# Performance work log

Hardware: AMD Instinct MI355X
Metric: run time of the kernel (lower is better)

The kernel has to match this reference:

```python
import jax, jax.numpy as jnp
import numpy as np

T = 4096          # flattened document length (tokens)
FLAT = 512        # 2 * lstm_hidden_size
HD = 256          # head embedding dim (head_emb + char_emb)
FEAT = 20         # feature_size
MAXW = 20         # max mention width
NCAND = 30000     # enumerated candidate spans
HID = 512         # scorer hidden size
K = 1638          # floor(T * ment_ratio=0.4)
C = 40            # max antecedents
DEPTH = 2         # coref_depth
NSPK = 10
MENT = 2 * FLAT + FEAT + HD        # 1300 mention emb size
BIN_WIDTHS = [1, 1, 1, 1, 1, 4, 8, 16, 32]   # sums to 65 -> covers clamp(dist,0,64)
BINS = jnp.asarray(np.concatenate([np.full(w, i, dtype=np.int32) for i, w in enumerate(BIN_WIDTHS)]))


def _scorer(x, w1, b1, w2, b2, w3, b3):
    h = jax.nn.relu(x @ w1 + b1)
    h = jax.nn.relu(h @ w2 + b2)
    return (h @ w3 + b3)[..., 0]


def setup_inputs():
    key = jax.random.key(0)
    ks = jax.random.split(key, 30)
    p = lambda i, s: jax.random.normal(ks[i], s, jnp.float32) * 0.02
    cand_starts = jax.random.randint(ks[25], (NCAND,), 0, T)
    widths = jax.random.randint(ks[26], (NCAND,), 0, MAXW)
    cand_ends = jnp.minimum(cand_starts + widths, T - 1)
    return {
        "flat_lstm_out": jax.random.normal(ks[0], (T, FLAT), jnp.float32),
        "head_doc_embs": jax.random.normal(ks[1], (T, HD), jnp.float32),
        "w_span_head": p(2, (FLAT,)), "b_span_head": jnp.zeros((), jnp.float32),
        "width_embed": p(3, (MAXW, FEAT)),
        "ms_w1": p(4, (MENT, HID)), "ms_b1": jnp.zeros((HID,), jnp.float32),
        "ms_w2": p(5, (HID, HID)), "ms_b2": jnp.zeros((HID,), jnp.float32),
        "ms_w3": p(6, (HID, 1)), "ms_b3": jnp.zeros((1,), jnp.float32),
        "fast_w": p(7, (MENT, MENT)), "fast_b": jnp.zeros((MENT,), jnp.float32),
        "ss_w1": p(8, (3 * MENT + 3 * FEAT, HID)), "ss_b1": jnp.zeros((HID,), jnp.float32),
        "ss_w2": p(9, (HID, HID)), "ss_b2": jnp.zeros((HID,), jnp.float32),
        "ss_w3": p(10, (HID, 1)), "ss_b3": jnp.zeros((1,), jnp.float32),
        "gate_w": p(11, (2 * MENT, MENT)), "gate_b": jnp.zeros((MENT,), jnp.float32),
        "speaker_embed": p(12, (2, FEAT)),
        "genre_embed": p(13, (7, FEAT)),
        "dist_embed": p(14, (len(BIN_WIDTHS), FEAT)),
        "cand_starts": cand_starts,
        "cand_ends": cand_ends,
        "speaker_ids": jax.random.randint(ks[27], (T,), 0, NSPK),
        "genre_id": 3,
    }


def reference(flat_lstm_out, head_doc_embs, w_span_head, b_span_head, width_embed,
              ms_w1, ms_b1, ms_w2, ms_b2, ms_w3, ms_b3, fast_w, fast_b,
              ss_w1, ss_b1, ss_w2, ss_b2, ss_w3, ss_b3, gate_w, gate_b,
              speaker_embed, genre_embed, dist_embed,
              cand_starts, cand_ends, speaker_ids, genre_id):
    neg = -jnp.inf
    # ---- mention (span) embeddings: start/end gather + width emb + attention-pooled head ----
    width = cand_ends - cand_starts + 1                              # [N]
    start_embs = flat_lstm_out[cand_starts]                          # [N,FLAT]
    end_embs = flat_lstm_out[cand_ends]                              # [N,FLAT]
    width_embs = width_embed[width - 1]                              # [N,FEAT]
    span_idxs = jnp.clip(jnp.arange(MAXW)[None, :] + cand_starts[:, None], 0, T - 1)  # [N,W]
    ment_doc = head_doc_embs[span_idxs]                              # [N,W,HD]
    head_scores = flat_lstm_out @ w_span_head + b_span_head          # [T]
    g = head_scores[span_idxs] + jnp.where(jnp.arange(MAXW)[None, :] < width[:, None], 0.0, neg)
    attn = jax.nn.softmax(g, axis=1)                                 # [N,W]
    head_embs = jnp.einsum('nw,nwd->nd', attn, ment_doc)             # [N,HD]
    cand_embs = jnp.concatenate([start_embs, end_embs, width_embs, head_embs], axis=1)  # [N,MENT]
    cand_scores = _scorer(cand_embs, ms_w1, ms_b1, ms_w2, ms_b2, ms_w3, ms_b3)          # [N]
    # ---- prune mentions: top-k by score, reordered by document position ----
    _, top_idx = jax.lax.top_k(cand_scores, K)
    ment_pos = cand_starts[top_idx] * cand_ends[-1] + cand_ends[top_idx]
    top_idx = top_idx[jnp.argsort(ment_pos)]
    ment_embs = cand_embs[top_idx]                                   # [K,MENT]
    ment_scores = cand_scores[top_idx]                               # [K]
    ment_speakers = speaker_ids[cand_starts[top_idx]]                # [K]
    # ---- fast (bilinear) antecedent scoring + top-c pruning ----
    idx = jnp.arange(K)
    mask = (idx[:, None] - idx[None, :]) > 0                         # antecedent must precede
    src = ment_embs @ fast_w + fast_b
    fast = src @ ment_embs.T + ment_scores[:, None] + ment_scores[None, :] + jnp.where(mask, 0.0, neg)
    top_fast, antes = jax.lax.top_k(fast, C)                         # [K,C]
    dummy = jnp.zeros((K, 1), fast.dtype)
    genre_emb = jnp.broadcast_to(genre_embed[genre_id][None, None, :], (K, C, FEAT))
    ante_scores = top_fast
    # ---- iterative slow antecedent scoring + gated refinement ----
    for _ in range(DEPTH):
        ante_ment = ment_embs[antes]                                 # [K,C,MENT]
        same = (ment_speakers[:, None] == ment_speakers[antes]).astype(jnp.int32)
        spk_emb = speaker_embed[same]                                # [K,C,FEAT]
        dist_bin = BINS[jnp.clip(idx[:, None] - antes, 0, 64)]
        dist_emb = dist_embed[dist_bin]                              # [K,C,FEAT]
        me = jnp.broadcast_to(ment_embs[:, None, :], (K, C, MENT))
        ante_emb = jnp.concatenate([me, ante_ment, ante_ment * me, spk_emb, genre_emb, dist_emb], axis=2)
        ante_scores = top_fast + _scorer(ante_emb, ss_w1, ss_b1, ss_w2, ss_b2, ss_w3, ss_b3)
        weights = jax.nn.softmax(jnp.concatenate([dummy, ante_scores], axis=1), axis=-1)  # [K,C+1]
        stacked = jnp.concatenate([ment_embs[:, None, :], ante_ment], axis=1)             # [K,C+1,MENT]
        attended = jnp.einsum('kc,kcd->kd', weights, stacked)
        f = jax.nn.sigmoid(jnp.concatenate([ment_embs, attended], axis=1) @ gate_w + gate_b)
        ment_embs = f * attended + (1.0 - f) * ment_embs
    return jnp.concatenate([dummy, ante_scores], axis=1)             # [K,C+1] coref logits
```

## Files before the change

kernel.cpp:

```cpp
#include <hip/hip_runtime.h>
#include <math.h>

#define T_LEN 4096
#define FLATD 512
#define HDD 256
#define FEATD 20
#define NCAND 30000
#define HIDD 512
#define KSEL 1638
#define CANT 40
#define MENTD 1300
#define KPAD 1312
#define NPAIR (KSEL*CANT)
#define NEG_INF (-__builtin_inff())

#define MF_RELU 1
#define MF_MASK 4
#define MF_GATE 8

typedef unsigned short u16;
typedef __attribute__((ext_vector_type(8))) short bf16x8;
typedef __attribute__((ext_vector_type(4))) float f32x4;

__device__ __forceinline__ unsigned ordf(float f){
  unsigned u = __float_as_uint(f);
  return (u & 0x80000000u) ? ~u : (u | 0x80000000u);
}
__device__ __forceinline__ float unordf(unsigned u){
  return __uint_as_float((u & 0x80000000u) ? (u ^ 0x80000000u) : ~u);
}
__device__ __forceinline__ float bf2f(u16 h){ return __uint_as_float(((unsigned)h) << 16); }
__device__ __forceinline__ u16 f2bf(float f){
  unsigned u = __float_as_uint(f);
  u += 0x7fffu + ((u >> 16) & 1u);
  return (u16)(u >> 16);
}
__device__ __forceinline__ unsigned pkmul(unsigned a, unsigned b){
  float a0 = __uint_as_float(a << 16), a1 = __uint_as_float(a & 0xffff0000u);
  float b0 = __uint_as_float(b << 16), b1 = __uint_as_float(b & 0xffff0000u);
  float p0 = a0*b0, p1 = a1*b1;
  unsigned r;
  asm("v_cvt_pk_bf16_f32 %0, %1, %2" : "=v"(r) : "v"(p0), "v"(p1));
  return r;
}
__device__ __forceinline__ int featsrc(int k){
  if (k < 1024) return k;
  if (k < 1280) return k + 20;
  if (k < 1300) return k - 256;
  return -1;
}
__device__ __forceinline__ int swz(int row, int k8){
  return row*32 + ((k8 ^ ((row >> 1) & 3)) << 3);
}
__device__ __forceinline__ void gload16(const u16* g, u16* l){
  __builtin_amdgcn_global_load_lds((const __attribute__((address_space(1))) void*)(g),
                                   (__attribute__((address_space(3))) void*)(l), 16, 0, 0);
}

__global__ __launch_bounds__(256) void k_prep(const float* __restrict__ flat,
    const float* __restrict__ wemb, const float* __restrict__ fast_b, const float* __restrict__ gate_b,
    u16* __restrict__ flatbf, u16* __restrict__ wembP, float* __restrict__ fbP, float* __restrict__ gbP)
{
  int i = blockIdx.x*256 + threadIdx.x;
  if (i < T_LEN*FLATD) flatbf[i] = f2bf(flat[i]);
  if (i < 20*32) wembP[i] = ((i & 31) < 20) ? f2bf(wemb[(i >> 5)*FEATD + (i & 31)]) : (u16)0;
  if (i < KPAD){
    int s = featsrc(i);
    fbP[i] = (s >= 0) ? fast_b[s] : 0.f;
    gbP[i] = (s >= 0) ? gate_b[s] : 0.f;
  }
}

__global__ __launch_bounds__(256) void k_head(const float* __restrict__ flat,
    const float* __restrict__ w, const float* __restrict__ b, float* __restrict__ hs)
{
  int lane = threadIdx.x & 63, wid = threadIdx.x >> 6;
  int row = blockIdx.x*4 + wid;
  if (row >= T_LEN) return;
  const float* x = flat + (size_t)row*FLATD;
  float s = 0.f;
  for (int j = lane; j < FLATD; j += 64) s += x[j]*w[j];
  #pragma unroll
  for (int o = 32; o; o >>= 1) s += __shfl_down(s, o, 64);
  if (lane == 0) hs[row] = s + b[0];
}

__global__ __launch_bounds__(256) void k_cand(const float* __restrict__ hs,
    const float* __restrict__ hdoc, const int* __restrict__ starts, const int* __restrict__ ends,
    u16* __restrict__ hemb)
{
  int wid = threadIdx.x >> 6, lane = threadIdx.x & 63;
  int n = blockIdx.x*4 + wid;
  if (n >= NCAND) return;
  int s = starts[n], e = ends[n];
  int width = e - s + 1;
  float g[20];
  #pragma unroll
  for (int w2 = 0; w2 < 20; ++w2) g[w2] = (w2 < width) ? hs[min(s + w2, T_LEN-1)] : NEG_INF;
  float m = NEG_INF;
  #pragma unroll
  for (int w2 = 0; w2 < 20; ++w2) m = fmaxf(m, g[w2]);
  float sum = 0.f;
  #pragma unroll
  for (int w2 = 0; w2 < 20; ++w2){ g[w2] = expf(g[w2] - m); sum += g[w2]; }
  float inv = 1.f/sum;
  #pragma unroll
  for (int di = 0; di < 4; ++di){
    int d = lane + di*64;
    float acc = 0.f;
    #pragma unroll
    for (int w2 = 0; w2 < 20; ++w2)
      acc += g[w2]*hdoc[(size_t)min(s + w2, T_LEN-1)*HDD + d];
    hemb[(size_t)n*HDD + d] = f2bf(acc*inv);
  }
}

__global__ __launch_bounds__(256) void k_transall(const float* __restrict__ ms_w1,
    const float* __restrict__ ms_w2, const float* __restrict__ fast_w,
    const float* __restrict__ ss_w1, const float* __restrict__ ss_w2,
    const float* __restrict__ gate_w,
    u16* ms1T, u16* ms2T, u16* fastT, u16* ss1abT, u16* sspT,
    u16* ss2T, u16* gateTall)
{
  const float* B; u16* D; int Kb, N, srcN, ldD, kperm, nperm;
  switch (blockIdx.z){
    case 0: B = ms_w1; D = ms1T; Kb = KPAD; N = HIDD; srcN = HIDD; ldD = KPAD; kperm = 1; nperm = 0; break;
    case 1: B = ms_w2; D = ms2T; Kb = HIDD; N = HIDD; srcN = HIDD; ldD = HIDD; kperm = 0; nperm = 0; break;
    case 2: B = fast_w; D = fastT; Kb = KPAD; N = MENTD; srcN = MENTD; ldD = KPAD; kperm = 1; nperm = 1; break;
    case 3: B = ss_w1; D = ss1abT; Kb = KPAD; N = HIDD; srcN = HIDD; ldD = KPAD; kperm = 1; nperm = 0; break;
    case 4: B = ss_w1 + (size_t)MENTD*HIDD; D = ss1abT + (size_t)512*KPAD; Kb = KPAD; N = HIDD; srcN = HIDD; ldD = KPAD; kperm = 1; nperm = 0; break;
    case 5: B = ss_w1 + (size_t)2*MENTD*HIDD; D = sspT; Kb = KPAD; N = HIDD; srcN = HIDD; ldD = KPAD; kperm = 1; nperm = 0; break;
    case 6: B = ss_w2; D = ss2T; Kb = HIDD; N = HIDD; srcN = HIDD; ldD = HIDD; kperm = 0; nperm = 0; break;
    case 7: B = gate_w; D = gateTall; Kb = KPAD; N = MENTD; srcN = MENTD; ldD = 2*KPAD; kperm = 1; nperm = 1; break;
    default: B = gate_w + (size_t)MENTD*MENTD; D = gateTall + KPAD; Kb = KPAD; N = MENTD; srcN = MENTD; ldD = 2*KPAD; kperm = 1; nperm = 1; break;
  }
  int k0 = blockIdx.x*32, n0 = blockIdx.y*32;
  if (k0 >= Kb || n0 >= N) return;
  __shared__ float t[32][33];
  int tx = threadIdx.x & 31, ty = threadIdx.x >> 5;
  for (int r = ty; r < 32; r += 8){
    int gk = k0 + r, gn = n0 + tx;
    int sk = kperm ? featsrc(gk) : ((gk < Kb) ? gk : -1);
    int sn = nperm ? ((gn < N) ? featsrc(gn) : -1) : ((gn < N) ? gn : -1);
    t[r][tx] = (sk >= 0 && sn >= 0) ? B[(size_t)sk*srcN + sn] : 0.f;
  }
  __syncthreads();
  for (int r = ty; r < 32; r += 8){
    int gn = n0 + r, gk = k0 + tx;
    if (gn < N && gk < Kb) D[(size_t)gn*ldD + gk] = f2bf(t[tx][r]);
  }
}

__global__ __launch_bounds__(256) void k_mfma_cand(
    const u16* __restrict__ flatbf, const u16* __restrict__ hemb, const u16* __restrict__ wembP,
    const int* __restrict__ starts, const int* __restrict__ ends,
    const u16* __restrict__ Bt, int M, const float* __restrict__ bias, u16* __restrict__ Cbf)
{
  __shared__ alignas(16) u16 As[4096];
  __shared__ alignas(16) u16 Bs[4096];
  int tid = threadIdx.x;
  int row0 = blockIdx.y*128, col0 = blockIdx.x*128;
  int lane = tid & 63, wid = tid >> 6;
  int wr = wid >> 1, wc = wid & 1;
  int l15 = lane & 15, l4 = lane >> 4;

  int s0 = tid, s1 = tid + 256;
  int r0s = s0 >> 2, c0s = s0 & 3;
  int r1s = s1 >> 2, c1s = s1 & 3;
  int k80 = (c0s ^ ((r0s >> 1) & 3)) << 3;
  int k81 = (c1s ^ ((r1s >> 1) & 3)) << 3;
  int n0r = row0 + r0s; if (n0r >= M) n0r = M - 1;
  int n1r = row0 + r1s; if (n1r >= M) n1r = M - 1;
  int sA0 = starts[n0r], eA0 = ends[n0r];
  int sA1 = starts[n1r], eA1 = ends[n1r];
  const u16* bS0 = flatbf + (size_t)sA0*FLATD;
  const u16* bE0 = flatbf + (size_t)eA0*FLATD;
  const u16* bH0 = hemb + (size_t)n0r*HDD;
  const u16* bW0 = wembP + (eA0 - sA0)*32;
  const u16* bS1 = flatbf + (size_t)sA1*FLATD;
  const u16* bE1 = flatbf + (size_t)eA1*FLATD;
  const u16* bH1p = hemb + (size_t)n1r*HDD;
  const u16* bW1 = wembP + (eA1 - sA1)*32;
  const u16* pb0 = Bt + (size_t)(col0 + r0s)*KPAD + k80;
  const u16* pb1 = Bt + (size_t)(col0 + r1s)*KPAD + k81;
  u16* la0 = As + s0*8; u16* la1 = As + s1*8;
  u16* lb0 = Bs + s0*8; u16* lb1 = Bs + s1*8;

  f32x4 acc[4][4];
  #pragma unroll
  for (int m = 0; m < 4; ++m)
    #pragma unroll
    for (int n = 0; n < 4; ++n)
      #pragma unroll
      for (int q = 0; q < 4; ++q) acc[m][n][q] = 0.f;

  for (int kt = 0; kt < KPAD/32; ++kt){
    int k0 = kt << 5;
    int f0 = k0 + k80, f1 = k0 + k81;
    const u16* src0 = (f0 < 512) ? bS0 + f0 : (f0 < 1024) ? bE0 + (f0 - 512)
                    : (f0 < 1280) ? bH0 + (f0 - 1024) : bW0 + (f0 - 1280);
    const u16* src1 = (f1 < 512) ? bS1 + f1 : (f1 < 1024) ? bE1 + (f1 - 512)
                    : (f1 < 1280) ? bH1p + (f1 - 1024) : bW1 + (f1 - 1280);
    gload16(src0, la0); gload16(src1, la1);
    gload16(pb0 + k0, lb0); gload16(pb1 + k0, lb1);
    __syncthreads();
    bf16x8 af[4], bfr[4];
    #pragma unroll
    for (int m = 0; m < 4; ++m){ int r = wr*64 + m*16 + l15; af[m] = *(const bf16x8*)(As + swz(r, l4)); }
    #pragma unroll
    for (int n = 0; n < 4; ++n){ int cc = wc*64 + n*16 + l15; bfr[n] = *(const bf16x8*)(Bs + swz(cc, l4)); }
    #pragma unroll
    for (int m = 0; m < 4; ++m)
      #pragma unroll
      for (int n = 0; n < 4; ++n)
        acc[m][n] = __builtin_amdgcn_mfma_f32_16x16x32_bf16(af[m], bfr[n], acc[m][n], 0, 0, 0);
    __syncthreads();
  }
  #pragma unroll
  for (int m = 0; m < 4; ++m){
    #pragma unroll
    for (int q = 0; q < 4; ++q){
      int grow = row0 + wr*64 + m*16 + l4*4 + q;
      if (grow >= M) continue;
      #pragma unroll
      for (int n = 0; n < 4; ++n){
        int gcol = col0 + wc*64 + n*16 + l15;
        float v = fmaxf(acc[m][n][q] + bias[gcol], 0.f);
        Cbf[(size_t)grow*HIDD + gcol] = f2bf(v);
      }
    }
  }
}

__global__ __launch_bounds__(256) void k_mfma(const u16* __restrict__ A,
    const u16* __restrict__ A2, const u16* __restrict__ Bt, int M, int N, int Kp, int ldA,
    const float* __restrict__ bias, const float* __restrict__ msc,
    float* __restrict__ Cf, int ldf, u16* __restrict__ Cbf, int ldbf, int Nstore, int flags,
    const u16* __restrict__ g_att, const u16* __restrict__ g_mo)
{
  __shared__ alignas(16) u16 As[4096];
  __shared__ alignas(16) u16 Bs[4096];
  int tid = threadIdx.x;
  int row0 = blockIdx.y*128, col0 = blockIdx.x*128;
  if ((flags & MF_MASK) && col0 >= row0 + 128) return;
  int lane = tid & 63, wid = tid >> 6;
  int wr = wid >> 1, wc = wid & 1;
  int l15 = lane & 15, l4 = lane >> 4;

  int s0 = tid, s1 = tid + 256;
  int r0s = s0 >> 2, c0s = s0 & 3;
  int r1s = s1 >> 2, c1s = s1 & 3;
  int k80 = (c0s ^ ((r0s >> 1) & 3)) << 3;
  int k81 = (c1s ^ ((r1s >> 1) & 3)) << 3;
  int ra0 = row0 + r0s; if (ra0 >= M) ra0 = M - 1;
  int ra1 = row0 + r1s; if (ra1 >= M) ra1 = M - 1;
  int cb0 = col0 + r0s; if (cb0 >= N) cb0 = N - 1;
  int cb1 = col0 + r1s; if (cb1 >= N) cb1 = N - 1;
  const u16* pa0 = A + (size_t)ra0*ldA + k80;
  const u16* pa1 = A + (size_t)ra1*ldA + k81;
  int kt1 = A2 ? (ldA >> 5) : (Kp >> 5);
  int koff = kt1 << 5;
  const u16* qa0 = A2 ? (A2 + (size_t)ra0*ldA + k80 - koff) : pa0;
  const u16* qa1 = A2 ? (A2 + (size_t)ra1*ldA + k81 - koff) : pa1;
  const u16* pb0 = Bt + (size_t)cb0*Kp + k80;
  const u16* pb1 = Bt + (size_t)cb1*Kp + k81;
  u16* la0 = As + s0*8; u16* la1 = As + s1*8;
  u16* lb0 = Bs + s0*8; u16* lb1 = Bs + s1*8;

  f32x4 acc[4][4];
  #pragma unroll
  for (int m = 0; m < 4; ++m)
    #pragma unroll
    for (int n = 0; n < 4; ++n)
      #pragma unroll
      for (int q = 0; q < 4; ++q) acc[m][n][q] = 0.f;

  int nkt = Kp >> 5;
  for (int kt = 0; kt < nkt; ++kt){
    int k0 = kt << 5;
    const u16* a0 = (kt < kt1) ? pa0 : qa0;
    const u16* a1 = (kt < kt1) ? pa1 : qa1;
    gload16(a0 + k0, la0); gload16(a1 + k0, la1);
    gload16(pb0 + k0, lb0); gload16(pb1 + k0, lb1);
    __syncthreads();
    bf16x8 af[4], bfr[4];
    #pragma unroll
    for (int m = 0; m < 4; ++m){ int r = wr*64 + m*16 + l15; af[m] = *(const bf16x8*)(As + swz(r, l4)); }
    #pragma unroll
    for (int n = 0; n < 4; ++n){ int cc = wc*64 + n*16 + l15; bfr[n] = *(const bf16x8*)(Bs + swz(cc, l4)); }
    #pragma unroll
    for (int m = 0; m < 4; ++m)
      #pragma unroll
      for (int n = 0; n < 4; ++n)
        acc[m][n] = __builtin_amdgcn_mfma_f32_16x16x32_bf16(af[m], bfr[n], acc[m][n], 0, 0, 0);
    __syncthreads();
  }
  #pragma unroll
  for (int m = 0; m < 4; ++m){
    #pragma unroll
    for (int q = 0; q < 4; ++q){
      int grow = row0 + wr*64 + m*16 + l4*4 + q;
      if (grow >= M) continue;
      #pragma unroll
      for (int n = 0; n < 4; ++n){
        int gcol = col0 + wc*64 + n*16 + l15;
        if (gcol < N){
          float v = acc[m][n][q];
          if (bias) v += bias[gcol];
          if (flags & MF_MASK){ v += msc[grow] + msc[gcol]; if (gcol >= grow) v = NEG_INF; }
          if (flags & MF_RELU) v = fmaxf(v, 0.f);
          if (flags & MF_GATE){
            float f = 1.f/(1.f + expf(-v));
            float res = f*bf2f(g_att[(size_t)grow*ldbf + gcol])
                      + (1.f - f)*bf2f(g_mo[(size_t)grow*ldbf + gcol]);
            Cbf[(size_t)grow*ldbf + gcol] = f2bf(res);
          } else {
            if (Cf)  Cf[(size_t)grow*ldf + gcol] = v;
            if (Cbf) Cbf[(size_t)grow*ldbf + gcol] = f2bf(v);
          }
        } else if (Cbf && gcol < Nstore){
          Cbf[(size_t)grow*ldbf + gcol] = 0;
        }
      }
    }
  }
}

__global__ __launch_bounds__(256) void k_mfma_rowdot(const u16* __restrict__ A,
    const u16* __restrict__ Bt, int M, const float* __restrict__ b2,
    const float* __restrict__ w3, const float* __restrict__ b3,
    const float* __restrict__ add, float* __restrict__ out)
{
  __shared__ alignas(16) u16 As[4096];
  __shared__ alignas(16) u16 Bs[4096];
  __shared__ float rsum[128][2];
  int tid = threadIdx.x;
  int row0 = blockIdx.x*128;
  int lane = tid & 63, wid = tid >> 6;
  int wr = wid >> 1, wc = wid & 1;
  int l15 = lane & 15, l4 = lane >> 4;

  int s0 = tid, s1 = tid + 256;
  int r0s = s0 >> 2, c0s = s0 & 3;
  int r1s = s1 >> 2, c1s = s1 & 3;
  int k80 = (c0s ^ ((r0s >> 1) & 3)) << 3;
  int k81 = (c1s ^ ((r1s >> 1) & 3)) << 3;
  int ra0 = row0 + r0s; if (ra0 >= M) ra0 = M - 1;
  int ra1 = row0 + r1s; if (ra1 >= M) ra1 = M - 1;
  const u16* pa0 = A + (size_t)ra0*HIDD + k80;
  const u16* pa1 = A + (size_t)ra1*HIDD + k81;
  u16* la0 = As + s0*8; u16* la1 = As + s1*8;
  u16* lb0 = Bs + s0*8; u16* lb1 = Bs + s1*8;

  float rd[4][4] = {};
  for (int p = 0; p < 4; ++p){
    int col0 = p*128;
    const u16* pb0 = Bt + (size_t)(col0 + r0s)*HIDD + k80;
    const u16* pb1 = Bt + (size_t)(col0 + r1s)*HIDD + k81;
    f32x4 acc[4][4];
    #pragma unroll
    for (int m = 0; m < 4; ++m)
      #pragma unroll
      for (int n = 0; n < 4; ++n)
        #pragma unroll
        for (int q = 0; q < 4; ++q) acc[m][n][q] = 0.f;
    for (int kt = 0; kt < HIDD/32; ++kt){
      int k0 = kt << 5;
      gload16(pa0 + k0, la0); gload16(pa1 + k0, la1);
      gload16(pb0 + k0, lb0); gload16(pb1 + k0, lb1);
      __syncthreads();
      bf16x8 af[4], bfr[4];
      #pragma unroll
      for (int m = 0; m < 4; ++m){ int r = wr*64 + m*16 + l15; af[m] = *(const bf16x8*)(As + swz(r, l4)); }
      #pragma unroll
      for (int n = 0; n < 4; ++n){ int cc = wc*64 + n*16 + l15; bfr[n] = *(const bf16x8*)(Bs + swz(cc, l4)); }
      #pragma unroll
      for (int m = 0; m < 4; ++m)
        #pragma unroll
        for (int n = 0; n < 4; ++n)
          acc[m][n] = __builtin_amdgcn_mfma_f32_16x16x32_bf16(af[m], bfr[n], acc[m][n], 0, 0, 0);
      __syncthreads();
    }
    #pragma unroll
    for (int n = 0; n < 4; ++n){
      int gcol = col0 + wc*64 + n*16 + l15;
      float bb = b2[gcol], ww = w3[gcol];
      #pragma unroll
      for (int m = 0; m < 4; ++m)
        #pragma unroll
        for (int q = 0; q < 4; ++q){
          float v = fmaxf(acc[m][n][q] + bb, 0.f);
          rd[m][q] = fmaf(v, ww, rd[m][q]);
        }
    }
  }
  #pragma unroll
  for (int m = 0; m < 4; ++m)
    #pragma unroll
    for (int q = 0; q < 4; ++q){
      float s = rd[m][q];
      s += __shfl_xor(s, 1, 64); s += __shfl_xor(s, 2, 64);
      s += __shfl_xor(s, 4, 64); s += __shfl_xor(s, 8, 64);
      if (l15 == 0) rsum[wr*64 + m*16 + l4*4 + q][wc] = s;
    }
  __syncthreads();
  if (tid < 128){
    int gr = row0 + tid;
    if (gr < M){
      float v = rsum[tid][0] + rsum[tid][1] + b3[0];
      if (add) v += add[gr];
      out[gr] = v;
    }
  }
}

__global__ __launch_bounds__(256) void k_d1_mfma(int Mc,
    const u16* __restrict__ ment, const int* __restrict__ antes, const int* __restrict__ mspk,
    const u16* __restrict__ Bt, const float* __restrict__ A_meb,
    const float* __restrict__ Svec, const float* __restrict__ Dvec, const float* __restrict__ cvec,
    u16* __restrict__ H1)
{
  __shared__ alignas(16) u16 As[4096];
  __shared__ alignas(16) u16 Bs[4096];
  __shared__ int ri[128], rj[128], rsame[128], rbin[128];
  int tid = threadIdx.x;
  int row0 = blockIdx.y*128, col0 = blockIdx.x*128;
  if (tid < 128){
    int r = row0 + tid;
    int p = (r < Mc ? r : 0);
    int i = p / CANT;
    int j = antes[p];
    ri[tid] = i; rj[tid] = j;
    rsame[tid] = (mspk[i] == mspk[j]) ? 1 : 0;
    int d = i - j; d = d < 0 ? 0 : (d > 64 ? 64 : d);
    rbin[tid] = (d <= 4) ? d : (d <= 8 ? 5 : (d <= 16 ? 6 : (d <= 32 ? 7 : 8)));
  }
  __syncthreads();
  int lane = tid & 63, wid = tid >> 6;
  int wr = wid >> 1, wc = wid & 1;
  int l15 = lane & 15, l4 = lane >> 4;

  int s0 = tid, s1 = tid + 256;
  int r0s = s0 >> 2, c0s = s0 & 3;
  int r1s = s1 >> 2, c1s = s1 & 3;
  int k80 = (c0s ^ ((r0s >> 1) & 3)) << 3;
  int k81 = (c1s ^ ((r1s >> 1) & 3)) << 3;
  const u16* pb0 = Bt + (size_t)(col0 + r0s)*KPAD + k80;
  const u16* pb1 = Bt + (size_t)(col0 + r1s)*KPAD + k81;
  u16* lb0 = Bs + s0*8; u16* lb1 = Bs + s1*8;
  const u16* pi0 = ment + (size_t)ri[r0s]*KPAD + k80;
  const u16* pj0 = ment + (size_t)rj[r0s]*KPAD + k80;
  const u16* pi1 = ment + (size_t)ri[r1s]*KPAD + k81;
  const u16* pj1 = ment + (size_t)rj[r1s]*KPAD + k81;

  f32x4 acc[4][4];
  #pragma unroll
  for (int m = 0; m < 4; ++m)
    #pragma unroll
    for (int n = 0; n < 4; ++n)
      #pragma unroll
      for (int q = 0; q < 4; ++q) acc[m][n][q] = 0.f;

  int nkt = KPAD >> 5;
  for (int kt = 0; kt < nkt; ++kt){
    int k0 = kt << 5;
    gload16(pb0 + k0, lb0); gload16(pb1 + k0, lb1);
    {
      uint4 va = *(const uint4*)(pi0 + k0);
      uint4 vb = *(const uint4*)(pj0 + k0);
      uint4 vo;
      vo.x = pkmul(va.x, vb.x); vo.y = pkmul(va.y, vb.y);
      vo.z = pkmul(va.z, vb.z); vo.w = pkmul(va.w, vb.w);
      *(uint4*)(As + s0*8) = vo;
      va = *(const uint4*)(pi1 + k0);
      vb = *(const uint4*)(pj1 + k0);
      vo.x = pkmul(va.x, vb.x); vo.y = pkmul(va.y, vb.y);
      vo.z = pkmul(va.z, vb.z); vo.w = pkmul(va.w, vb.w);
      *(uint4*)(As + s1*8) = vo;
    }
    __syncthreads();
    bf16x8 af[4], bfr[4];
    #pragma unroll
    for (int m = 0; m < 4; ++m){ int r = wr*64 + m*16 + l15; af[m] = *(const bf16x8*)(As + swz(r, l4)); }
    #pragma unroll
    for (int n = 0; n < 4; ++n){ int cc = wc*64 + n*16 + l15; bfr[n] = *(const bf16x8*)(Bs + swz(cc, l4)); }
    #pragma unroll
    for (int m = 0; m < 4; ++m)
      #pragma unroll
      for (int n = 0; n < 4; ++n)
        acc[m][n] = __builtin_amdgcn_mfma_f32_16x16x32_bf16(af[m], bfr[n], acc[m][n], 0, 0, 0);
    __syncthreads();
  }
  #pragma unroll
  for (int m = 0; m < 4; ++m){
    #pragma unroll
    for (int q = 0; q < 4; ++q){
      int rl = wr*64 + m*16 + l4*4 + q;
      int grow = row0 + rl;
      if (grow >= Mc) continue;
      const float* me = A_meb + (size_t)ri[rl]*1024;
      const float* an = A_meb + (size_t)rj[rl]*1024 + 512;
      const float* sv = Svec + rsame[rl]*HIDD;
      const float* dv = Dvec + rbin[rl]*HIDD;
      #pragma unroll
      for (int n = 0; n < 4; ++n){
        int gcol = col0 + wc*64 + n*16 + l15;
        float v = acc[m][n][q] + me[gcol] + an[gcol] + sv[gcol] + dv[gcol] + cvec[gcol];
        H1[(size_t)grow*HIDD + gcol] = f2bf(fmaxf(v, 0.f));
      }
    }
  }
}

__global__ __launch_bounds__(256) void k_selzero(unsigned* selws){
  int i = blockIdx.x*256 + threadIdx.x;
  if (i < 6156) selws[i] = 0;
}
__global__ __launch_bounds__(256) void k_hist(const float* __restrict__ scores,
    unsigned* __restrict__ selws, int pass)
{
  int n = blockIdx.x*256 + threadIdx.x;
  if (n >= NCAND) return;
  unsigned u = ordf(scores[n]);
  const unsigned* meta = selws + 6144;
  if (pass == 0) atomicAdd(&selws[u >> 21], 1u);
  else if (pass == 1){ if ((u >> 21) == meta[0]) atomicAdd(&selws[2048 + ((u >> 10) & 0x7FFu)], 1u); }
  else { if ((u >> 10) == meta[2]) atomicAdd(&selws[4096 + (u & 0x3FFu)], 1u); }
}
__global__ __launch_bounds__(1024) void k_thresh(unsigned* __restrict__ selws, int mode){
  __shared__ unsigned a[2048], b[2048];
  int tid = threadIdx.x;
  unsigned* meta = selws + 6144;
  const unsigned* gbin = selws + (mode == 0 ? 0 : (mode == 1 ? 2048 : 4096));
  unsigned target = (mode == 0) ? (unsigned)KSEL : meta[mode == 1 ? 1 : 3];
  a[tid] = gbin[tid]; a[tid + 1024] = gbin[tid + 1024];
  unsigned *src = a, *dst = b;
  for (int step = 1; step < 2048; step <<= 1){
    __syncthreads();
    for (int i = tid; i < 2048; i += 1024)
      dst[i] = src[i] + ((i + step < 2048) ? src[i + step] : 0u);
    unsigned* t2 = src; src = dst; dst = t2;
  }
  __syncthreads();
  for (int i = tid; i < 2048; i += 1024){
    unsigned si = src[i], sn = (i < 2047) ? src[i+1] : 0u;
    if (si >= target && sn < target){
      if (mode == 0){ meta[0] = (unsigned)i; meta[1] = target - sn; }
      else if (mode == 1){ meta[2] = (meta[0] << 11) | (unsigned)i; meta[3] = target - sn; }
      else { meta[4] = (meta[2] << 10) | (unsigned)i; meta[5] = target - sn; }
    }
  }
}
__global__ __launch_bounds__(256) void k_compact(const float* __restrict__ scores,
    unsigned* __restrict__ selws, int* __restrict__ g_sel, unsigned* __restrict__ g_eq)
{
  int n = blockIdx.x*256 + threadIdx.x;
  if (n >= NCAND) return;
  unsigned kth = selws[6144 + 4];
  unsigned* cnt = selws + 6152;
  unsigned u = ordf(scores[n]);
  if (u > kth){ unsigned p = atomicAdd(&cnt[0], 1u); g_sel[p] = n; }
  else if (u == kth){ unsigned p = atomicAdd(&cnt[1], 1u); if (p < 1024) g_eq[p] = (unsigned)n; }
}
__global__ __launch_bounds__(1024) void k_eqrank(unsigned* __restrict__ selws,
    const unsigned* __restrict__ g_eq, int* __restrict__ g_sel)
{
  __shared__ unsigned eq[1024];
  int tid = threadIdx.x;
  unsigned neq = selws[6152 + 1]; if (neq > 1024u) neq = 1024u;
  unsigned E = selws[6144 + 5];
  unsigned G = selws[6152 + 0];
  eq[tid] = (tid < (int)neq) ? g_eq[tid] : 0xFFFFFFFFu;
  __syncthreads();
  if (tid < (int)neq){
    unsigned mine = eq[tid]; unsigned r = 0;
    for (unsigned j = 0; j < neq; ++j) r += (eq[j] < mine) ? 1u : 0u;
    if (r < E) g_sel[G + r] = (int)mine;
  }
}
__global__ __launch_bounds__(256) void k_rank1(const float* __restrict__ scores,
    const int* __restrict__ g_sel, int* __restrict__ ranked)
{
  __shared__ unsigned long long key[KSEL];
  int tid = threadIdx.x;
  for (int t = tid; t < KSEL; t += 256){
    int n = g_sel[t];
    key[t] = ((unsigned long long)(~ordf(scores[n])) << 32) | (unsigned)n;
  }
  __syncthreads();
  int t = blockIdx.x*256 + tid;
  if (t >= KSEL) return;
  unsigned long long mine = key[t];
  int r = 0;
  #pragma unroll 16
  for (int j = 0; j < KSEL; ++j) r += (key[j] < mine) ? 1 : 0;
  ranked[r] = (int)(mine & 0xFFFFFFFFu);
}
__global__ __launch_bounds__(256) void k_rank2(const int* __restrict__ ranked,
    const int* __restrict__ starts, const int* __restrict__ ends, int* __restrict__ top_idx)
{
  __shared__ unsigned long long key[KSEL];
  int tid = threadIdx.x;
  int elast = ends[NCAND-1];
  for (int t = tid; t < KSEL; t += 256){
    int n = ranked[t];
    unsigned mp = (unsigned)(starts[n]*elast + ends[n]);
    key[t] = ((unsigned long long)mp << 11) | (unsigned)t;
  }
  __syncthreads();
  int t = blockIdx.x*256 + tid;
  if (t >= KSEL) return;
  unsigned long long mine = key[t];
  int r = 0;
  #pragma unroll 16
  for (int j = 0; j < KSEL; ++j) r += (key[j] < mine) ? 1 : 0;
  top_idx[r] = ranked[t];
}

__global__ __launch_bounds__(256) void k_gather(const int* __restrict__ top_idx,
    const u16* __restrict__ flatbf, const u16* __restrict__ hemb, const u16* __restrict__ wembP,
    const int* __restrict__ starts, const int* __restrict__ ends,
    const float* __restrict__ cscores, const int* __restrict__ spk_ids,
    u16* __restrict__ ment, float* __restrict__ mscore, int* __restrict__ mspk)
{
  int k = blockIdx.x; int n = top_idx[k];
  int s = starts[n], e = ends[n];
  int v = threadIdx.x;
  if (v < KPAD/8){
    int f0 = v*8;
    const u16* src = (f0 < 512) ? flatbf + (size_t)s*FLATD + f0
                   : (f0 < 1024) ? flatbf + (size_t)e*FLATD + (f0 - 512)
                   : (f0 < 1280) ? hemb + (size_t)n*HDD + (f0 - 1024)
                   : wembP + (e - s)*32 + (f0 - 1280);
    *(uint4*)(ment + (size_t)k*KPAD + f0) = *(const uint4*)src;
  }
  if (threadIdx.x == 0){ mscore[k] = cscores[n]; mspk[k] = spk_ids[s]; }
}

__global__ __launch_bounds__(256) void k_f3(const float* __restrict__ fast,
    float* __restrict__ top_fast, int* __restrict__ antes)
{
  int wid = threadIdx.x >> 6, lane = threadIdx.x & 63;
  int i = blockIdx.x*4 + wid;
  if (i >= KSEL) return;
  const float* row = fast + (size_t)i*KSEL;
  unsigned long long key[26];
  #pragma unroll
  for (int t = 0; t < 26; ++t){
    int j = lane + (t << 6);
    unsigned long long k2 = 0ULL;
    if (j < i) k2 = ((unsigned long long)ordf(row[j]) << 32) | (unsigned)(0xFFFFFFFFu - (unsigned)j);
    key[t] = k2;
  }
  for (int c = 0; c < CANT; ++c){
    unsigned long long m = 0ULL;
    #pragma unroll
    for (int t = 0; t < 26; ++t) if (key[t] > m) m = key[t];
    #pragma unroll
    for (int o = 32; o; o >>= 1){
      unsigned long long v = __shfl_xor(m, o, 64);
      if (v > m) m = v;
    }
    if (m){
      #pragma unroll
      for (int t = 0; t < 26; ++t) if (key[t] == m) key[t] = 0ULL;
    }
    if (lane == 0){
      if (m){
        top_fast[(size_t)i*CANT + c] = unordf((unsigned)(m >> 32));
        antes[(size_t)i*CANT + c]    = (int)(0xFFFFFFFFu - (unsigned)(m & 0xFFFFFFFFu));
      } else {
        top_fast[(size_t)i*CANT + c] = NEG_INF;
        antes[(size_t)i*CANT + c]    = c;
      }
    }
  }
}

__global__ __launch_bounds__(256) void k_dsmall(const float* __restrict__ ss_w1,
    const float* __restrict__ ss_b1, const float* __restrict__ spk_emb,
    const float* __restrict__ gen_emb, const float* __restrict__ dist_emb,
    const int* __restrict__ genre_id, float* __restrict__ Svec, float* __restrict__ Dvec,
    float* __restrict__ cvec)
{
  int r = blockIdx.x;
  for (int h = threadIdx.x; h < HIDD; h += 256){
    const float* e; const float* wb; float acc;
    if (r < 2){ e = spk_emb + r*FEATD; wb = ss_w1 + (size_t)3900*HIDD; acc = 0.f; }
    else if (r < 11){ e = dist_emb + (r-2)*FEATD; wb = ss_w1 + (size_t)3940*HIDD; acc = 0.f; }
    else { e = gen_emb + genre_id[0]*FEATD; wb = ss_w1 + (size_t)3920*HIDD; acc = ss_b1[h]; }
    for (int f = 0; f < FEATD; ++f) acc += e[f]*wb[(size_t)f*HIDD + h];
    if (r < 2) Svec[r*HIDD + h] = acc;
    else if (r < 11) Dvec[(r-2)*HIDD + h] = acc;
    else cvec[h] = acc;
  }
}

__global__ __launch_bounds__(256) void k_d4a(const float* __restrict__ ante_sc,
    const int* __restrict__ antes, const u16* __restrict__ ment, u16* __restrict__ att_bf)
{
  int i = blockIdx.x;
  __shared__ float w[CANT+1];
  __shared__ int aj[CANT];
  if (threadIdx.x == 0){
    float s[CANT]; float m = 0.f;
    #pragma unroll
    for (int c = 0; c < CANT; ++c){ s[c] = ante_sc[i*CANT + c]; m = fmaxf(m, s[c]); }
    float e0 = expf(0.f - m);
    float sum = e0;
    float ex[CANT];
    #pragma unroll
    for (int c = 0; c < CANT; ++c){ ex[c] = expf(s[c] - m); sum += ex[c]; }
    float inv = 1.f/sum;
    w[0] = e0*inv;
    #pragma unroll
    for (int c = 0; c < CANT; ++c) w[c+1] = ex[c]*inv;
  }
  if (threadIdx.x < CANT) aj[threadIdx.x] = antes[i*CANT + threadIdx.x];
  __syncthreads();
  for (int d = threadIdx.x; d < KPAD; d += 256){
    if (d < MENTD){
      float acc = w[0]*bf2f(ment[(size_t)i*KPAD + d]);
      for (int c = 0; c < CANT; ++c) acc += w[c+1]*bf2f(ment[(size_t)aj[c]*KPAD + d]);
      att_bf[(size_t)i*KPAD + d] = f2bf(acc);
    } else att_bf[(size_t)i*KPAD + d] = 0;
  }
}

__global__ __launch_bounds__(256) void k_out(const float* __restrict__ ante_sc, float* __restrict__ out){
  int idx = blockIdx.x*256 + threadIdx.x;
  if (idx >= KSEL*41) return;
  int i = idx / 41, c = idx % 41;
  float v = (c == 0) ? 0.f : ante_sc[i*CANT + (c-1)];
  if (!isfinite(v)) v = -3.0e38f;
  out[idx] = v;
}

__global__ void k_zero(float* out, int n){
  int i = blockIdx.x*256 + threadIdx.x;
  if (i < n) out[i] = 0.f;
}

extern "C" void kernel_launch(void* const* d_in, const int* in_sizes, int n_in,
                              void* d_out, int out_size, void* d_ws, size_t ws_size,
                              hipStream_t stream)
{
  const float* flat   = (const float*)d_in[0];
  const float* hdoc   = (const float*)d_in[1];
  const float* w_head = (const float*)d_in[2];
  const float* b_head = (const float*)d_in[3];
  const float* wemb   = (const float*)d_in[4];
  const float* ms_w1  = (const float*)d_in[5];
  const float* ms_b1  = (const float*)d_in[6];
  const float* ms_w2  = (const float*)d_in[7];
  const float* ms_b2  = (const float*)d_in[8];
  const float* ms_w3  = (const float*)d_in[9];
  const float* ms_b3  = (const float*)d_in[10];
  const float* fast_w = (const float*)d_in[11];
  const float* fast_b = (const float*)d_in[12];
  const float* ss_w1  = (const float*)d_in[13];
  const float* ss_b1  = (const float*)d_in[14];
  const float* ss_w2  = (const float*)d_in[15];
  const float* ss_b2  = (const float*)d_in[16];
  const float* ss_w3  = (const float*)d_in[17];
  const float* ss_b3  = (const float*)d_in[18];
  const float* gate_w = (const float*)d_in[19];
  const float* gate_b = (const float*)d_in[20];
  const float* spk_e  = (const float*)d_in[21];
  const float* gen_e  = (const float*)d_in[22];
  const float* dist_e = (const float*)d_in[23];
  const int* starts   = (const int*)d_in[24];
  const int* ends     = (const int*)d_in[25];
  const int* spk_ids  = (const int*)d_in[26];
  const int* genre_id = (const int*)d_in[27];
  float* out = (float*)d_out;

  size_t off = 0;
  char* base = (char*)d_ws;
  auto alloc = [&](size_t nbytes) -> void* {
    void* p = (void*)(base + off);
    off += ((nbytes + 255)/256)*256;
    return p;
  };
  float* head_sc = (float*)alloc((size_t)T_LEN*4);
  u16*   flatbf  = (u16*)alloc((size_t)T_LEN*FLATD*2);
  u16*   wembP   = (u16*)alloc((size_t)20*32*2);
  float* fbP     = (float*)alloc((size_t)KPAD*4);
  float* gbP     = (float*)alloc((size_t)KPAD*4);
  u16*   hemb    = (u16*)alloc((size_t)NCAND*HDD*2);
  float* cscores = (float*)alloc((size_t)NCAND*4);
  int*   top_idx = (int*)alloc(2048*4);
  unsigned* selws= (unsigned*)alloc(6160*4);
  int*   g_sel   = (int*)alloc((size_t)KSEL*4);
  unsigned* g_eq = (unsigned*)alloc(1024*4);
  int*   g_rank  = (int*)alloc((size_t)KSEL*4);
  u16*   ms1T    = (u16*)alloc((size_t)HIDD*KPAD*2);
  u16*   ms2T    = (u16*)alloc((size_t)HIDD*HIDD*2);
  u16*   fastT   = (u16*)alloc((size_t)MENTD*KPAD*2);
  u16*   ss1abT  = (u16*)alloc((size_t)1024*KPAD*2);
  u16*   sspT    = (u16*)alloc((size_t)HIDD*KPAD*2);
  u16*   ss2T    = (u16*)alloc((size_t)HIDD*HIDD*2);
  u16*   gateTall= (u16*)alloc((size_t)MENTD*2*KPAD*2);
  u16*   ment    = (u16*)alloc((size_t)KSEL*KPAD*2);
  u16*   mentB   = (u16*)alloc((size_t)KSEL*KPAD*2);
  u16*   srcb    = (u16*)alloc((size_t)KSEL*KPAD*2);
  float* mscore  = (float*)alloc((size_t)KSEL*4);
  int*   mspk    = (int*)alloc((size_t)KSEL*4);
  float* fastm   = (float*)alloc((size_t)KSEL*KSEL*4);
  float* top_fast= (float*)alloc((size_t)NPAIR*4);
  int*   antes   = (int*)alloc((size_t)NPAIR*4);
  float* ante_sc = (float*)alloc((size_t)NPAIR*4);
  float* A_meb   = (float*)alloc((size_t)KSEL*1024*4);
  float* Svec    = (float*)alloc(2*HIDD*4);
  float* Dvec    = (float*)alloc(9*HIDD*4);
  float* cvec    = (float*)alloc(HIDD*4);
  u16*   att_bf  = (u16*)alloc((size_t)KSEL*KPAD*2);
  u16*   bufH1   = (u16*)alloc((size_t)NPAIR*HIDD*2);

  if (ws_size < off){
    k_zero<<<(KSEL*41 + 255)/256, 256, 0, stream>>>(out, KSEL*41);
    return;
  }

  k_prep<<<(T_LEN*FLATD + 255)/256, 256, 0, stream>>>(flat, wemb, fast_b, gate_b,
                                                      flatbf, wembP, fbP, gbP);
  k_transall<<<dim3(KPAD/32, 41, 9), 256, 0, stream>>>(ms_w1, ms_w2, fast_w, ss_w1, ss_w2, gate_w,
      ms1T, ms2T, fastT, ss1abT, sspT, ss2T, gateTall);

  k_head<<<T_LEN/4, 256, 0, stream>>>(flat, w_head, b_head, head_sc);
  k_cand<<<NCAND/4, 256, 0, stream>>>(head_sc, hdoc, starts, ends, hemb);

  k_mfma_cand<<<dim3(HIDD/128, (NCAND + 127)/128), 256, 0, stream>>>(
      flatbf, hemb, wembP, starts, ends, ms1T, NCAND, ms_b1, bufH1);
  k_mfma_rowdot<<<(NCAND + 127)/128, 256, 0, stream>>>(bufH1, ms2T, NCAND, ms_b2, ms_w3, ms_b3,
                                                       nullptr, cscores);

  k_selzero<<<25, 256, 0, stream>>>(selws);
  k_hist<<<(NCAND + 255)/256, 256, 0, stream>>>(cscores, selws, 0);
  k_thresh<<<1, 1024, 0, stream>>>(selws, 0);
  k_hist<<<(NCAND + 255)/256, 256, 0, stream>>>(cscores, selws, 1);
  k_thresh<<<1, 1024, 0, stream>>>(selws, 1);
  k_hist<<<(NCAND + 255)/256, 256, 0, stream>>>(cscores, selws, 2);
  k_thresh<<<1, 1024, 0, stream>>>(selws, 2);
  k_compact<<<(NCAND + 255)/256, 256, 0, stream>>>(cscores, selws, g_sel, g_eq);
  k_eqrank<<<1, 1024, 0, stream>>>(selws, g_eq, g_sel);
  k_rank1<<<(KSEL + 255)/256, 256, 0, stream>>>(cscores, g_sel, g_rank);
  k_rank2<<<(KSEL + 255)/256, 256, 0, stream>>>(g_rank, starts, ends, top_idx);

  k_gather<<<KSEL, 256, 0, stream>>>(top_idx, flatbf, hemb, wembP, starts, ends, cscores, spk_ids,
                                     ment, mscore, mspk);

  k_mfma<<<dim3((MENTD+127)/128, (KSEL+127)/128), 256, 0, stream>>>(
      ment, nullptr, fastT, KSEL, MENTD, KPAD, KPAD, fbP, nullptr,
      nullptr, 0, srcb, KPAD, KPAD, 0, nullptr, nullptr);
  k_mfma<<<dim3((KSEL+127)/128, (KSEL+127)/128), 256, 0, stream>>>(
      srcb, nullptr, ment, KSEL, KSEL, KPAD, KPAD, nullptr, mscore,
      fastm, KSEL, nullptr, 0, 0, MF_MASK, nullptr, nullptr);
  k_f3<<<(KSEL+3)/4, 256, 0, stream>>>(fastm, top_fast, antes);

  k_dsmall<<<12, 256, 0, stream>>>(ss_w1, ss_b1, spk_e, gen_e, dist_e, genre_id, Svec, Dvec, cvec);

  const u16* mcur = ment;
  for (int iter = 0; iter < 2; ++iter){
    k_mfma<<<dim3(8, (KSEL+127)/128), 256, 0, stream>>>(
        mcur, nullptr, ss1abT, KSEL, 1024, KPAD, KPAD, nullptr, nullptr,
        A_meb, 1024, nullptr, 0, 0, 0, nullptr, nullptr);
    k_d1_mfma<<<dim3(HIDD/128, (NPAIR + 127)/128), 256, 0, stream>>>(
        NPAIR, mcur, antes, mspk, sspT, A_meb, Svec, Dvec, cvec, bufH1);
    k_mfma_rowdot<<<(NPAIR + 127)/128, 256, 0, stream>>>(bufH1, ss2T, NPAIR, ss_b2, ss_w3, ss_b3,
                                                         top_fast, ante_sc);
    if (iter == 0){
      k_d4a<<<KSEL, 256, 0, stream>>>(ante_sc, antes, mcur, att_bf);
      k_mfma<<<dim3((MENTD+127)/128, (KSEL+127)/128), 256, 0, stream>>>(
          ment, att_bf, gateTall, KSEL, MENTD, 2*KPAD, KPAD, gbP, nullptr,
          nullptr, 0, mentB, KPAD, KPAD, MF_GATE, att_bf, ment);
      mcur = mentB;
    }
  }

  k_out<<<(KSEL*41 + 255)/256, 256, 0, stream>>>(ante_sc, out);
}
```

Before: 1.357 ms.

## Widen pair GEMM tile, prefetch gathers, precombine feature biases, vectorize attention

```diff
diff --git a/kernel.cpp b/kernel.cpp
--- a/kernel.cpp
+++ b/kernel.cpp
@@ -59,7 +59,8 @@
 
 __global__ __launch_bounds__(256) void k_prep(const float* __restrict__ flat,
     const float* __restrict__ wemb, const float* __restrict__ fast_b, const float* __restrict__ gate_b,
-    u16* __restrict__ flatbf, u16* __restrict__ wembP, float* __restrict__ fbP, float* __restrict__ gbP)
+    u16* __restrict__ flatbf, u16* __restrict__ wembP, float* __restrict__ fbP, float* __restrict__ gbP,
+    unsigned* __restrict__ selws)
 {
   int i = blockIdx.x*256 + threadIdx.x;
   if (i < T_LEN*FLATD) flatbf[i] = f2bf(flat[i]);
@@ -69,6 +70,7 @@
     fbP[i] = (s >= 0) ? fast_b[s] : 0.f;
     gbP[i] = (s >= 0) ? gate_b[s] : 0.f;
   }
+  if (i < 6156) selws[i] = 0;
 }
 
 __global__ __launch_bounds__(256) void k_head(const float* __restrict__ flat,
@@ -417,23 +419,24 @@
 __global__ __launch_bounds__(256) void k_d1_mfma(int Mc,
     const u16* __restrict__ ment, const int* __restrict__ antes, const int* __restrict__ mspk,
     const u16* __restrict__ Bt, const float* __restrict__ A_meb,
-    const float* __restrict__ Svec, const float* __restrict__ Dvec, const float* __restrict__ cvec,
-    u16* __restrict__ H1)
+    const float* __restrict__ comb, u16* __restrict__ H1)
 {
   __shared__ alignas(16) u16 As[4096];
-  __shared__ alignas(16) u16 Bs[4096];
-  __shared__ int ri[128], rj[128], rsame[128], rbin[128];
+  __shared__ alignas(16) u16 Bs[8192];
+  __shared__ int ri[128], rj[128], rcomb[128];
   int tid = threadIdx.x;
-  int row0 = blockIdx.y*128, col0 = blockIdx.x*128;
+  int row0 = blockIdx.y*128;
+  int col0 = blockIdx.x*256;
   if (tid < 128){
     int r = row0 + tid;
     int p = (r < Mc ? r : 0);
     int i = p / CANT;
     int j = antes[p];
     ri[tid] = i; rj[tid] = j;
-    rsame[tid] = (mspk[i] == mspk[j]) ? 1 : 0;
+    int same = (mspk[i] == mspk[j]) ? 1 : 0;
     int d = i - j; d = d < 0 ? 0 : (d > 64 ? 64 : d);
-    rbin[tid] = (d <= 4) ? d : (d <= 8 ? 5 : (d <= 16 ? 6 : (d <= 32 ? 7 : 8)));
+    int bin = (d <= 4) ? d : (d <= 8 ? 5 : (d <= 16 ? 6 : (d <= 32 ? 7 : 8)));
+    rcomb[tid] = same*9 + bin;
   }
   __syncthreads();
   int lane = tid & 63, wid = tid >> 6;
@@ -445,50 +448,67 @@
   int r1s = s1 >> 2, c1s = s1 & 3;
   int k80 = (c0s ^ ((r0s >> 1) & 3)) << 3;
   int k81 = (c1s ^ ((r1s >> 1) & 3)) << 3;
-  const u16* pb0 = Bt + (size_t)(col0 + r0s)*KPAD + k80;
-  const u16* pb1 = Bt + (size_t)(col0 + r1s)*KPAD + k81;
-  u16* lb0 = Bs + s0*8; u16* lb1 = Bs + s1*8;
   const u16* pi0 = ment + (size_t)ri[r0s]*KPAD + k80;
   const u16* pj0 = ment + (size_t)rj[r0s]*KPAD + k80;
   const u16* pi1 = ment + (size_t)ri[r1s]*KPAD + k81;
   const u16* pj1 = ment + (size_t)rj[r1s]*KPAD + k81;
-
-  f32x4 acc[4][4];
+  int t0 = tid, t1 = tid + 256, t2 = tid + 512, t3 = tid + 768;
+  int rB0 = t0 >> 2, rB1 = t1 >> 2, rB2 = t2 >> 2, rB3 = t3 >> 2;
+  int kB0 = ((t0 & 3) ^ ((rB0 >> 1) & 3)) << 3;
+  int kB1 = ((t1 & 3) ^ ((rB1 >> 1) & 3)) << 3;
+  int kB2 = ((t2 & 3) ^ ((rB2 >> 1) & 3)) << 3;
+  int kB3 = ((t3 & 3) ^ ((rB3 >> 1) & 3)) << 3;
+  const u16* pb0 = Bt + (size_t)(col0 + rB0)*KPAD + kB0;
+  const u16* pb1 = Bt + (size_t)(col0 + rB1)*KPAD + kB1;
+  const u16* pb2 = Bt + (size_t)(col0 + rB2)*KPAD + kB2;
+  const u16* pb3 = Bt + (size_t)(col0 + rB3)*KPAD + kB3;
+
+  f32x4 acc[4][8];
   #pragma unroll
   for (int m = 0; m < 4; ++m)
     #pragma unroll
-    for (int n = 0; n < 4; ++n)
+    for (int n = 0; n < 8; ++n)
       #pragma unroll
       for (int q = 0; q < 4; ++q) acc[m][n][q] = 0.f;
+
+  uint4 va0 = *(const uint4*)pi0;
+  uint4 vb0 = *(const uint4*)pj0;
+  uint4 va1 = *(const uint4*)pi1;
+  uint4 vb1 = *(const uint4*)pj1;
 
   int nkt = KPAD >> 5;
   for (int kt = 0; kt < nkt; ++kt){
     int k0 = kt << 5;
-    gload16(pb0 + k0, lb0); gload16(pb1 + k0, lb1);
     {
-      uint4 va = *(const uint4*)(pi0 + k0);
-      uint4 vb = *(const uint4*)(pj0 + k0);
       uint4 vo;
-      vo.x = pkmul(va.x, vb.x); vo.y = pkmul(va.y, vb.y);
-      vo.z = pkmul(va.z, vb.z); vo.w = pkmul(va.w, vb.w);
+      vo.x = pkmul(va0.x, vb0.x); vo.y = pkmul(va0.y, vb0.y);
+      vo.z = pkmul(va0.z, vb0.z); vo.w = pkmul(va0.w, vb0.w);
       *(uint4*)(As + s0*8) = vo;
-      va = *(const uint4*)(pi1 + k0);
-      vb = *(const uint4*)(pj1 + k0);
-      vo.x = pkmul(va.x, vb.x); vo.y = pkmul(va.y, vb.y);
-      vo.z = pkmul(va.z, vb.z); vo.w = pkmul(va.w, vb.w);
+      vo.x = pkmul(va1.x, vb1.x); vo.y = pkmul(va1.y, vb1.y);
+      vo.z = pkmul(va1.z, vb1.z); vo.w = pkmul(va1.w, vb1.w);
       *(uint4*)(As + s1*8) = vo;
     }
+    gload16(pb0 + k0, Bs + t0*8); gload16(pb1 + k0, Bs + t1*8);
+    gload16(pb2 + k0, Bs + t2*8); gload16(pb3 + k0, Bs + t3*8);
+    if (kt + 1 < nkt){
+      int kn = (kt + 1) << 5;
+      va0 = *(const uint4*)(pi0 + kn);
+      vb0 = *(const uint4*)(pj0 + kn);
+      va1 = *(const uint4*)(pi1 + kn);
+      vb1 = *(const uint4*)(pj1 + kn);
+    }
     __syncthreads();
-    bf16x8 af[4], bfr[4];
+    bf16x8 af[4];
     #pragma unroll
     for (int m = 0; m < 4; ++m){ int r = wr*64 + m*16 + l15; af[m] = *(const bf16x8*)(As + swz(r, l4)); }
     #pragma unroll
-    for (int n = 0; n < 4; ++n){ int cc = wc*64 + n*16 + l15; bfr[n] = *(const bf16x8*)(Bs + swz(cc, l4)); }
-    #pragma unroll
-    for (int m = 0; m < 4; ++m)
-      #pragma unroll
-      for (int n = 0; n < 4; ++n)
-        acc[m][n] = __builtin_amdgcn_mfma_f32_16x16x32_bf16(af[m], bfr[n], acc[m][n], 0, 0, 0);
+    for (int n = 0; n < 8; ++n){
+      int cc = wc*128 + n*16 + l15;
+      bf16x8 bfr = *(const bf16x8*)(Bs + swz(cc, l4));
+      #pragma unroll
+      for (int m = 0; m < 4; ++m)
+        acc[m][n] = __builtin_amdgcn_mfma_f32_16x16x32_bf16(af[m], bfr, acc[m][n], 0, 0, 0);
+    }
     __syncthreads();
   }
   #pragma unroll
@@ -500,22 +520,17 @@
       if (grow >= Mc) continue;
       const float* me = A_meb + (size_t)ri[rl]*1024;
       const float* an = A_meb + (size_t)rj[rl]*1024 + 512;
-      const float* sv = Svec + rsame[rl]*HIDD;
-      const float* dv = Dvec + rbin[rl]*HIDD;
-      #pragma unroll
-      for (int n = 0; n < 4; ++n){
-        int gcol = col0 + wc*64 + n*16 + l15;
-        float v = acc[m][n][q] + me[gcol] + an[gcol] + sv[gcol] + dv[gcol] + cvec[gcol];
+      const float* cb = comb + (size_t)rcomb[rl]*HIDD;
+      #pragma unroll
+      for (int n = 0; n < 8; ++n){
+        int gcol = col0 + wc*128 + n*16 + l15;
+        float v = acc[m][n][q] + me[gcol] + an[gcol] + cb[gcol];
         H1[(size_t)grow*HIDD + gcol] = f2bf(fmaxf(v, 0.f));
       }
     }
   }
 }
 
-__global__ __launch_bounds__(256) void k_selzero(unsigned* selws){
-  int i = blockIdx.x*256 + threadIdx.x;
-  if (i < 6156) selws[i] = 0;
-}
 __global__ __launch_bounds__(256) void k_hist(const float* __restrict__ scores,
     unsigned* __restrict__ selws, int pass)
 {
@@ -680,19 +695,24 @@
 __global__ __launch_bounds__(256) void k_dsmall(const float* __restrict__ ss_w1,
     const float* __restrict__ ss_b1, const float* __restrict__ spk_emb,
     const float* __restrict__ gen_emb, const float* __restrict__ dist_emb,
-    const int* __restrict__ genre_id, float* __restrict__ Svec, float* __restrict__ Dvec,
-    float* __restrict__ cvec)
+    const int* __restrict__ genre_id, float* __restrict__ comb)
 {
   int r = blockIdx.x;
+  int same = r / 9, bin = r % 9;
+  const float* es = spk_emb + same*FEATD;
+  const float* eg = gen_emb + genre_id[0]*FEATD;
+  const float* ed = dist_emb + bin*FEATD;
   for (int h = threadIdx.x; h < HIDD; h += 256){
-    const float* e; const float* wb; float acc;
-    if (r < 2){ e = spk_emb + r*FEATD; wb = ss_w1 + (size_t)3900*HIDD; acc = 0.f; }
-    else if (r < 11){ e = dist_emb + (r-2)*FEATD; wb = ss_w1 + (size_t)3940*HIDD; acc = 0.f; }
-    else { e = gen_emb + genre_id[0]*FEATD; wb = ss_w1 + (size_t)3920*HIDD; acc = ss_b1[h]; }
-    for (int f = 0; f < FEATD; ++f) acc += e[f]*wb[(size_t)f*HIDD + h];
-    if (r < 2) Svec[r*HIDD + h] = acc;
-    else if (r < 11) Dvec[(r-2)*HIDD + h] = acc;
-    else cvec[h] = acc;
+    float acc = ss_b1[h];
+    const float* ws_ = ss_w1 + (size_t)3900*HIDD + h;
+    const float* wg  = ss_w1 + (size_t)3920*HIDD + h;
+    const float* wd  = ss_w1 + (size_t)3940*HIDD + h;
+    for (int f = 0; f < FEATD; ++f){
+      acc += es[f]*ws_[(size_t)f*HIDD];
+      acc += eg[f]*wg[(size_t)f*HIDD];
+      acc += ed[f]*wd[(size_t)f*HIDD];
+    }
+    comb[(size_t)r*HIDD + h] = acc;
   }
 }
 
@@ -718,13 +738,34 @@
   }
   if (threadIdx.x < CANT) aj[threadIdx.x] = antes[i*CANT + threadIdx.x];
   __syncthreads();
-  for (int d = threadIdx.x; d < KPAD; d += 256){
-    if (d < MENTD){
-      float acc = w[0]*bf2f(ment[(size_t)i*KPAD + d]);
-      for (int c = 0; c < CANT; ++c) acc += w[c+1]*bf2f(ment[(size_t)aj[c]*KPAD + d]);
-      att_bf[(size_t)i*KPAD + d] = f2bf(acc);
-    } else att_bf[(size_t)i*KPAD + d] = 0;
-  }
+  int v = threadIdx.x;
+  if (v >= KPAD/8) return;
+  int d0 = v*8;
+  float r[8] = {};
+  {
+    uint4 x = *(const uint4*)(ment + (size_t)i*KPAD + d0);
+    float w0 = w[0];
+    const unsigned* px = (const unsigned*)&x;
+    #pragma unroll
+    for (int h = 0; h < 4; ++h){
+      r[2*h]   = w0*__uint_as_float(px[h] << 16);
+      r[2*h+1] = w0*__uint_as_float(px[h] & 0xffff0000u);
+    }
+  }
+  for (int c = 0; c < CANT; ++c){
+    uint4 x = *(const uint4*)(ment + (size_t)aj[c]*KPAD + d0);
+    float wc_ = w[c+1];
+    const unsigned* px = (const unsigned*)&x;
+    #pragma unroll
+    for (int h = 0; h < 4; ++h){
+      r[2*h]   = fmaf(wc_, __uint_as_float(px[h] << 16), r[2*h]);
+      r[2*h+1] = fmaf(wc_, __uint_as_float(px[h] & 0xffff0000u), r[2*h+1]);
+    }
+  }
+  u16 o[8];
+  #pragma unroll
+  for (int h = 0; h < 8; ++h) o[h] = f2bf(r[h]);
+  *(uint4*)(att_bf + (size_t)i*KPAD + d0) = *(const uint4*)o;
 }
 
 __global__ __launch_bounds__(256) void k_out(const float* __restrict__ ante_sc, float* __restrict__ out){
@@ -811,9 +852,7 @@
   int*   antes   = (int*)alloc((size_t)NPAIR*4);
   float* ante_sc = (float*)alloc((size_t)NPAIR*4);
   float* A_meb   = (float*)alloc((size_t)KSEL*1024*4);
-  float* Svec    = (float*)alloc(2*HIDD*4);
-  float* Dvec    = (float*)alloc(9*HIDD*4);
-  float* cvec    = (float*)alloc(HIDD*4);
+  float* comb    = (float*)alloc((size_t)18*HIDD*4);
   u16*   att_bf  = (u16*)alloc((size_t)KSEL*KPAD*2);
   u16*   bufH1   = (u16*)alloc((size_t)NPAIR*HIDD*2);
 
@@ -823,7 +862,7 @@
   }
 
   k_prep<<<(T_LEN*FLATD + 255)/256, 256, 0, stream>>>(flat, wemb, fast_b, gate_b,
-                                                      flatbf, wembP, fbP, gbP);
+                                                      flatbf, wembP, fbP, gbP, selws);
   k_transall<<<dim3(KPAD/32, 41, 9), 256, 0, stream>>>(ms_w1, ms_w2, fast_w, ss_w1, ss_w2, gate_w,
       ms1T, ms2T, fastT, ss1abT, sspT, ss2T, gateTall);
 
@@ -835,7 +874,6 @@
   k_mfma_rowdot<<<(NCAND + 127)/128, 256, 0, stream>>>(bufH1, ms2T, NCAND, ms_b2, ms_w3, ms_b3,
                                                        nullptr, cscores);
 
-  k_selzero<<<25, 256, 0, stream>>>(selws);
   k_hist<<<(NCAND + 255)/256, 256, 0, stream>>>(cscores, selws, 0);
   k_thresh<<<1, 1024, 0, stream>>>(selws, 0);
   k_hist<<<(NCAND + 255)/256, 256, 0, stream>>>(cscores, selws, 1);
@@ -858,15 +896,15 @@
       fastm, KSEL, nullptr, 0, 0, MF_MASK, nullptr, nullptr);
   k_f3<<<(KSEL+3)/4, 256, 0, stream>>>(fastm, top_fast, antes);
 
-  k_dsmall<<<12, 256, 0, stream>>>(ss_w1, ss_b1, spk_e, gen_e, dist_e, genre_id, Svec, Dvec, cvec);
+  k_dsmall<<<18, 256, 0, stream>>>(ss_w1, ss_b1, spk_e, gen_e, dist_e, genre_id, comb);
 
   const u16* mcur = ment;
   for (int iter = 0; iter < 2; ++iter){
     k_mfma<<<dim3(8, (KSEL+127)/128), 256, 0, stream>>>(
         mcur, nullptr, ss1abT, KSEL, 1024, KPAD, KPAD, nullptr, nullptr,
         A_meb, 1024, nullptr, 0, 0, 0, nullptr, nullptr);
-    k_d1_mfma<<<dim3(HIDD/128, (NPAIR + 127)/128), 256, 0, stream>>>(
-        NPAIR, mcur, antes, mspk, sspT, A_meb, Svec, Dvec, cvec, bufH1);
+    k_d1_mfma<<<dim3(2, (NPAIR + 127)/128), 256, 0, stream>>>(
+        NPAIR, mcur, antes, mspk, sspT, A_meb, comb, bufH1);
     k_mfma_rowdot<<<(NPAIR + 127)/128, 256, 0, stream>>>(bufH1, ss2T, NPAIR, ss_b2, ss_w3, ss_b3,
                                                          top_fast, ante_sc);
     if (iter == 0){
```

After: 1.262 ms. 7.0% less time.
